# Kernel tuning notes

Hardware: AMD Instinct MI355X
Metric: run time of the kernel (lower is better)

## Reference

```python
import jax, jax.numpy as jnp
import numpy as np

TOPK_POS = 16
TOPK_NEG = 16
EPS = 1e-12  # F.normalize default eps


def _l2norm(x):
    # torch.nn.functional.normalize(p=2, dim=1): x / max(||x||_2, eps)
    n = jnp.sqrt(jnp.sum(x * x, axis=1, keepdims=True))
    return x / jnp.maximum(n, EPS)


def setup_inputs() -> dict:
    key = jax.random.key(0)
    k0, k1, k2, k3, k4 = jax.random.split(key, 5)
    B, I, J, C = 32, 1024, 2048, 1024
    f_rad = jax.random.normal(k0, (B, I), dtype=jnp.float32)
    f_histo = jax.random.normal(k1, (B, J), dtype=jnp.float32)
    rad_mask = jax.random.randint(k2, (B,), 0, 2).astype(bool)
    histo_mask = jax.random.randint(k3, (B,), 0, 2).astype(bool)
    # nn.Linear(in_channels*2, out_channels): weight [C, 2*I], bias [C]
    W = jax.random.normal(k4, (C, 2 * I), dtype=jnp.float32) / np.sqrt(2 * I)
    b = jnp.zeros((C,), dtype=jnp.float32)
    token = jnp.zeros((1, C), dtype=jnp.float32)  # missing_modality_token
    return {"f_rad": f_rad, "f_histo": f_histo, "rad_mask": rad_mask,
            "histo_mask": histo_mask, "W": W, "b": b, "token": token}


def reference(f_rad, f_histo, rad_mask, histo_mask, W, b, token):
    r = _l2norm(f_rad)            # [B, I]
    h = _l2norm(f_histo)          # [B, J]
    sim = jnp.einsum('bi,bj->bij', r, h)  # [B, I, J]
    pos_map = jnp.mean(jax.lax.top_k(sim, TOPK_POS)[0], axis=-1)    # [B, I]
    neg_map = jnp.mean(jax.lax.top_k(-sim, TOPK_NEG)[0], axis=-1)   # [B, I]
    # cat([B,1,I],[B,1,I], dim=1).view(B,-1) == concat(pos, neg) along features
    feat = jnp.concatenate([pos_map, neg_map], axis=1)  # [B, 2I]
    emb = feat @ W.T + b                                 # [B, C]
    # modality_flags = ~torch.min(rad_mask, histo_mask)  (bool AND then NOT)
    flags = (~(rad_mask & histo_mask)).astype(emb.dtype)[:, None]  # [B, 1]
    return emb + token * flags
```

## Files before the change

kernel.cpp:

```cpp
#include <hip/hip_runtime.h>
#include <math.h>

#define NB 32
#define NI 1024
#define NJ 2048
#define NC 1024
#define K2 2048

__global__ __launch_bounds__(256)
void prep_kernel(const float* __restrict__ f_rad,
                 const float* __restrict__ f_histo,
                 const unsigned char* __restrict__ rad_mask,
                 const unsigned char* __restrict__ histo_mask,
                 const float* __restrict__ bias,
                 const float* __restrict__ token,
                 float* __restrict__ F,
                 float* __restrict__ out)
{
    __shared__ float hb[NJ];
    __shared__ float lists[256][16];
    __shared__ float red[256];
    __shared__ float sc[4];

    const int b = blockIdx.x;
    const int t = threadIdx.x;

    float ss = 0.f;
#pragma unroll
    for (int i = 0; i < NJ / 256; ++i) {
        float v = f_histo[b * NJ + t + i * 256];
        hb[t + i * 256] = v;
        ss += v * v;
    }
    red[t] = ss;
    __syncthreads();
#pragma unroll
    for (int s = 128; s > 0; s >>= 1) {
        if (t < s) red[t] += red[t + s];
        __syncthreads();
    }
    if (t == 0) sc[0] = fmaxf(sqrtf(red[0]), 1e-12f);

    for (int pass = 0; pass < 2; ++pass) {
        const float sgn = pass ? -1.f : 1.f;
        float v[16];
#pragma unroll
        for (int i = 0; i < 8; ++i) v[i] = sgn * hb[t + i * 256];
#pragma unroll
        for (int i = 8; i < 16; ++i) v[i] = -__builtin_inff();

#pragma unroll
        for (int a = 0; a < 7; ++a)
#pragma unroll
            for (int c = 0; c < 7 - a; ++c) {
                float x = v[c], y = v[c + 1];
                v[c] = fmaxf(x, y);
                v[c + 1] = fminf(x, y);
            }

        __syncthreads();
#pragma unroll
        for (int i = 0; i < 16; ++i) lists[t][i] = v[i];
        __syncthreads();

#pragma unroll
        for (int s = 128; s >= 1; s >>= 1) {
            if (t < s) {
                float w[16], m[16];
#pragma unroll
                for (int i = 0; i < 16; ++i) w[i] = lists[t + s][i];
#pragma unroll
                for (int i = 0; i < 16; ++i) m[i] = fmaxf(v[i], w[15 - i]);
#pragma unroll
                for (int st = 8; st >= 1; st >>= 1)
#pragma unroll
                    for (int i = 0; i < 16; ++i)
                        if ((i & st) == 0) {
                            float x = m[i], y = m[i + st];
                            m[i] = fmaxf(x, y);
                            m[i + st] = fminf(x, y);
                        }
#pragma unroll
                for (int i = 0; i < 16; ++i) { v[i] = m[i]; lists[t][i] = m[i]; }
            }
            __syncthreads();
        }
        if (t == 0) {
            float s16 = 0.f;
#pragma unroll
            for (int i = 0; i < 16; ++i) s16 += v[i];
            sc[1 + pass] = s16;
        }
    }

    float rv[4];
    float ss2 = 0.f;
#pragma unroll
    for (int i = 0; i < 4; ++i) {
        rv[i] = f_rad[b * NI + t + i * 256];
        ss2 += rv[i] * rv[i];
    }
    __syncthreads();
    red[t] = ss2;
    __syncthreads();
#pragma unroll
    for (int s = 128; s > 0; s >>= 1) {
        if (t < s) red[t] += red[t + s];
        __syncthreads();
    }
    if (t == 0) sc[3] = fmaxf(sqrtf(red[0]), 1e-12f);
    __syncthreads();

    const float hnorm = sc[0];
    const float Hpos = sc[1] / (16.f * hnorm);
    const float Hneg = -sc[2] / (16.f * hnorm);
    const float rnorm = sc[3];

#pragma unroll
    for (int i = 0; i < 4; ++i) {
        float rn = rv[i] / rnorm;
        float p, q;
        if (rn > 0.f) { p = rn * Hpos;  q = -rn * Hneg; }
        else          { p = rn * Hneg;  q = -rn * Hpos; }
        F[b * K2 + t + i * 256]      = p;
        F[b * K2 + NI + t + i * 256] = q;
    }

    const float flag = (rad_mask[b] != 0 && histo_mask[b] != 0) ? 0.f : 1.f;
#pragma unroll
    for (int i = 0; i < NC / 256; ++i) {
        int c = t + i * 256;
        out[b * NC + c] = bias[c] + token[c] * flag;
    }
}

__global__ __launch_bounds__(256)
void gemm_kernel(const float* __restrict__ F,
                 const float* __restrict__ W,
                 float* __restrict__ out)
{
    __shared__ __align__(16) float Fs[NB][512];

    const int t = threadIdx.x;
    const int k0 = blockIdx.y * 1024;
    const int wave = t >> 6;
    const int lane = t & 63;
    const int c0 = blockIdx.x * 8 + wave * 2;

    float acc0[32], acc1[32];
#pragma unroll
    for (int b = 0; b < 32; ++b) { acc0[b] = 0.f; acc1[b] = 0.f; }

    const float4* Wr0 = reinterpret_cast<const float4*>(W + (size_t)c0 * K2 + k0);
    const float4* Wr1 = reinterpret_cast<const float4*>(W + (size_t)(c0 + 1) * K2 + k0);

    for (int ch = 0; ch < 2; ++ch) {
        const int kbase = k0 + ch * 512;
#pragma unroll
        for (int f = 0; f < 16; ++f) {
            int idx = t + f * 256;
            int row = idx >> 7;
            int col = idx & 127;
            reinterpret_cast<float4*>(&Fs[row][0])[col] =
                reinterpret_cast<const float4*>(F + row * K2 + kbase)[col];
        }
        __syncthreads();

#pragma unroll
        for (int r = 0; r < 2; ++r) {
            const int kk4 = r * 64 + lane;
            float4 w0 = Wr0[ch * 128 + kk4];
            float4 w1 = Wr1[ch * 128 + kk4];
#pragma unroll
            for (int b = 0; b < 32; ++b) {
                float4 fv = reinterpret_cast<const float4*>(&Fs[b][0])[kk4];
                acc0[b] = fmaf(fv.x, w0.x, acc0[b]);
                acc0[b] = fmaf(fv.y, w0.y, acc0[b]);
                acc0[b] = fmaf(fv.z, w0.z, acc0[b]);
                acc0[b] = fmaf(fv.w, w0.w, acc0[b]);
                acc1[b] = fmaf(fv.x, w1.x, acc1[b]);
                acc1[b] = fmaf(fv.y, w1.y, acc1[b]);
                acc1[b] = fmaf(fv.z, w1.z, acc1[b]);
                acc1[b] = fmaf(fv.w, w1.w, acc1[b]);
            }
        }
        __syncthreads();
    }

#pragma unroll
    for (int b = 0; b < 32; ++b) {
#pragma unroll
        for (int off = 32; off >= 1; off >>= 1) {
            acc0[b] += __shfl_xor(acc0[b], off, 64);
            acc1[b] += __shfl_xor(acc1[b], off, 64);
        }
    }

    float myval = 0.f;
    const int bsel = lane >> 1;
    const int csel = lane & 1;
#pragma unroll
    for (int b = 0; b < 32; ++b)
        if (bsel == b) myval = csel ? acc1[b] : acc0[b];

    atomicAdd(&out[bsel * NC + c0 + csel], myval);
}

extern "C" void kernel_launch(void* const* d_in, const int* in_sizes, int n_in,
                              void* d_out, int out_size, void* d_ws, size_t ws_size,
                              hipStream_t stream) {
    const float* f_rad       = (const float*)d_in[0];
    const float* f_histo     = (const float*)d_in[1];
    const unsigned char* rm  = (const unsigned char*)d_in[2];
    const unsigned char* hm  = (const unsigned char*)d_in[3];
    const float* W           = (const float*)d_in[4];
    const float* bias        = (const float*)d_in[5];
    const float* token       = (const float*)d_in[6];
    float* out = (float*)d_out;
    float* F   = (float*)d_ws;

    prep_kernel<<<NB, 256, 0, stream>>>(f_rad, f_histo, rm, hm, bias, token, F, out);
    dim3 grid(128, 2);
    gemm_kernel<<<grid, 256, 0, stream>>>(F, W, out);
}
```

Baseline: 101.8 us.

## Fuse top-k passes, use wave-shuffle reductions, drop LDS staging in GEMM

The prep kernel now sorts and merges the positive and negative top-16 lists in one tree pass instead of two. Norm reductions use wave shuffles plus a 4-entry shared array, which removes long chains of __syncthreads. The GEMM kernel no longer stages F in shared memory and reads it straight from global/cache, and the cross-lane reduction uses a butterfly combine that halves the shuffle count. These changes aim to cut barrier and shuffle overhead, at the cost of more register pressure and uncached-through-LDS global reads of F.

```diff
diff --git a/kernel.cpp b/kernel.cpp
--- a/kernel.cpp
+++ b/kernel.cpp
@@ -6,6 +6,24 @@
 #define NJ 2048
 #define NC 1024
 #define K2 2048
+
+__device__ __forceinline__ void merge16(float* __restrict__ v,
+                                        const float* __restrict__ w) {
+    float m[16];
+#pragma unroll
+    for (int i = 0; i < 16; ++i) m[i] = fmaxf(v[i], w[15 - i]);
+#pragma unroll
+    for (int st = 8; st >= 1; st >>= 1)
+#pragma unroll
+        for (int i = 0; i < 16; ++i)
+            if ((i & st) == 0) {
+                float x = m[i], y = m[i + st];
+                m[i] = fmaxf(x, y);
+                m[i + st] = fminf(x, y);
+            }
+#pragma unroll
+    for (int i = 0; i < 16; ++i) v[i] = m[i];
+}
 
 __global__ __launch_bounds__(256)
 void prep_kernel(const float* __restrict__ f_rad,
@@ -17,81 +35,66 @@
                  float* __restrict__ F,
                  float* __restrict__ out)
 {
-    __shared__ float hb[NJ];
-    __shared__ float lists[256][16];
-    __shared__ float red[256];
-    __shared__ float sc[4];
+    __shared__ float listsP[256][16];
+    __shared__ float listsN[256][16];
+    __shared__ float red[4];
 
     const int b = blockIdx.x;
     const int t = threadIdx.x;
-
+    const int wave = t >> 6, lane = t & 63;
+
+    float hv[8];
     float ss = 0.f;
 #pragma unroll
-    for (int i = 0; i < NJ / 256; ++i) {
-        float v = f_histo[b * NJ + t + i * 256];
-        hb[t + i * 256] = v;
-        ss += v * v;
-    }
-    red[t] = ss;
-    __syncthreads();
-#pragma unroll
-    for (int s = 128; s > 0; s >>= 1) {
-        if (t < s) red[t] += red[t + s];
+    for (int i = 0; i < 8; ++i) {
+        hv[i] = f_histo[b * NJ + t + i * 256];
+        ss += hv[i] * hv[i];
+    }
+#pragma unroll
+    for (int off = 1; off < 64; off <<= 1) ss += __shfl_xor(ss, off, 64);
+    if (lane == 0) red[wave] = ss;
+
+    float vp[16], vn[16];
+#pragma unroll
+    for (int i = 0; i < 8; ++i) { vp[i] = hv[i]; vn[i] = -hv[i]; }
+#pragma unroll
+    for (int i = 8; i < 16; ++i) { vp[i] = -INFINITY; vn[i] = -INFINITY; }
+#pragma unroll
+    for (int a = 0; a < 7; ++a)
+#pragma unroll
+        for (int c = 0; c < 7 - a; ++c) {
+            float x = vp[c], y = vp[c + 1];
+            vp[c] = fmaxf(x, y); vp[c + 1] = fminf(x, y);
+            x = vn[c]; y = vn[c + 1];
+            vn[c] = fmaxf(x, y); vn[c + 1] = fminf(x, y);
+        }
+
+    __syncthreads();
+    const float hnorm = fmaxf(sqrtf(red[0] + red[1] + red[2] + red[3]), 1e-12f);
+
+#pragma unroll
+    for (int i = 0; i < 16; ++i) { listsP[t][i] = vp[i]; listsN[t][i] = vn[i]; }
+    __syncthreads();
+
+#pragma unroll
+    for (int s = 128; s >= 1; s >>= 1) {
+        if (t < s) {
+            float wp[16], wn[16];
+#pragma unroll
+            for (int i = 0; i < 16; ++i) { wp[i] = listsP[t + s][i]; wn[i] = listsN[t + s][i]; }
+            merge16(vp, wp);
+            merge16(vn, wn);
+#pragma unroll
+            for (int i = 0; i < 16; ++i) { listsP[t][i] = vp[i]; listsN[t][i] = vn[i]; }
+        }
         __syncthreads();
     }
-    if (t == 0) sc[0] = fmaxf(sqrtf(red[0]), 1e-12f);
-
-    for (int pass = 0; pass < 2; ++pass) {
-        const float sgn = pass ? -1.f : 1.f;
-        float v[16];
-#pragma unroll
-        for (int i = 0; i < 8; ++i) v[i] = sgn * hb[t + i * 256];
-#pragma unroll
-        for (int i = 8; i < 16; ++i) v[i] = -__builtin_inff();
-
-#pragma unroll
-        for (int a = 0; a < 7; ++a)
-#pragma unroll
-            for (int c = 0; c < 7 - a; ++c) {
-                float x = v[c], y = v[c + 1];
-                v[c] = fmaxf(x, y);
-                v[c + 1] = fminf(x, y);
-            }
-
-        __syncthreads();
-#pragma unroll
-        for (int i = 0; i < 16; ++i) lists[t][i] = v[i];
-        __syncthreads();
-
-#pragma unroll
-        for (int s = 128; s >= 1; s >>= 1) {
-            if (t < s) {
-                float w[16], m[16];
-#pragma unroll
-                for (int i = 0; i < 16; ++i) w[i] = lists[t + s][i];
-#pragma unroll
-                for (int i = 0; i < 16; ++i) m[i] = fmaxf(v[i], w[15 - i]);
-#pragma unroll
-                for (int st = 8; st >= 1; st >>= 1)
-#pragma unroll
-                    for (int i = 0; i < 16; ++i)
-                        if ((i & st) == 0) {
-                            float x = m[i], y = m[i + st];
-                            m[i] = fmaxf(x, y);
-                            m[i + st] = fminf(x, y);
-                        }
-#pragma unroll
-                for (int i = 0; i < 16; ++i) { v[i] = m[i]; lists[t][i] = m[i]; }
-            }
-            __syncthreads();
-        }
-        if (t == 0) {
-            float s16 = 0.f;
-#pragma unroll
-            for (int i = 0; i < 16; ++i) s16 += v[i];
-            sc[1 + pass] = s16;
-        }
-    }
+
+    float sumP = 0.f, sumN = 0.f;
+#pragma unroll
+    for (int i = 0; i < 16; ++i) { sumP += listsP[0][i]; sumN += listsN[0][i]; }
+    const float Hpos = sumP / (16.f * hnorm);
+    const float Hneg = -sumN / (16.f * hnorm);
 
     float rv[4];
     float ss2 = 0.f;
@@ -100,21 +103,12 @@
         rv[i] = f_rad[b * NI + t + i * 256];
         ss2 += rv[i] * rv[i];
     }
-    __syncthreads();
-    red[t] = ss2;
-    __syncthreads();
-#pragma unroll
-    for (int s = 128; s > 0; s >>= 1) {
-        if (t < s) red[t] += red[t + s];
-        __syncthreads();
-    }
-    if (t == 0) sc[3] = fmaxf(sqrtf(red[0]), 1e-12f);
-    __syncthreads();
-
-    const float hnorm = sc[0];
-    const float Hpos = sc[1] / (16.f * hnorm);
-    const float Hneg = -sc[2] / (16.f * hnorm);
-    const float rnorm = sc[3];
+#pragma unroll
+    for (int off = 1; off < 64; off <<= 1) ss2 += __shfl_xor(ss2, off, 64);
+    __syncthreads();
+    if (lane == 0) red[wave] = ss2;
+    __syncthreads();
+    const float rnorm = fmaxf(sqrtf(red[0] + red[1] + red[2] + red[3]), 1e-12f);
 
 #pragma unroll
     for (int i = 0; i < 4; ++i) {
@@ -135,75 +129,58 @@
 }
 
 __global__ __launch_bounds__(256)
-void gemm_kernel(const float* __restrict__ F,
+void gemm_kernel(const float4* __restrict__ F4,
                  const float* __restrict__ W,
                  float* __restrict__ out)
 {
-    __shared__ __align__(16) float Fs[NB][512];
-
     const int t = threadIdx.x;
-    const int k0 = blockIdx.y * 1024;
-    const int wave = t >> 6;
-    const int lane = t & 63;
+    const int wave = t >> 6, lane = t & 63;
     const int c0 = blockIdx.x * 8 + wave * 2;
+    const int kb4 = blockIdx.y * 256;
 
     float acc0[32], acc1[32];
 #pragma unroll
     for (int b = 0; b < 32; ++b) { acc0[b] = 0.f; acc1[b] = 0.f; }
 
-    const float4* Wr0 = reinterpret_cast<const float4*>(W + (size_t)c0 * K2 + k0);
-    const float4* Wr1 = reinterpret_cast<const float4*>(W + (size_t)(c0 + 1) * K2 + k0);
-
-    for (int ch = 0; ch < 2; ++ch) {
-        const int kbase = k0 + ch * 512;
-#pragma unroll
-        for (int f = 0; f < 16; ++f) {
-            int idx = t + f * 256;
-            int row = idx >> 7;
-            int col = idx & 127;
-            reinterpret_cast<float4*>(&Fs[row][0])[col] =
-                reinterpret_cast<const float4*>(F + row * K2 + kbase)[col];
+    const float4* Wr0 = reinterpret_cast<const float4*>(W + (size_t)c0 * K2) + kb4;
+    const float4* Wr1 = reinterpret_cast<const float4*>(W + (size_t)(c0 + 1) * K2) + kb4;
+
+#pragma unroll
+    for (int r = 0; r < 4; ++r) {
+        const int kk4 = r * 64 + lane;
+        float4 w0 = Wr0[kk4];
+        float4 w1 = Wr1[kk4];
+#pragma unroll
+        for (int b = 0; b < 32; ++b) {
+            float4 fv = F4[b * 512 + kb4 + kk4];
+            acc0[b] = fmaf(fv.x, w0.x, acc0[b]);
+            acc0[b] = fmaf(fv.y, w0.y, acc0[b]);
+            acc0[b] = fmaf(fv.z, w0.z, acc0[b]);
+            acc0[b] = fmaf(fv.w, w0.w, acc0[b]);
+            acc1[b] = fmaf(fv.x, w1.x, acc1[b]);
+            acc1[b] = fmaf(fv.y, w1.y, acc1[b]);
+            acc1[b] = fmaf(fv.z, w1.z, acc1[b]);
+            acc1[b] = fmaf(fv.w, w1.w, acc1[b]);
         }
-        __syncthreads();
-
-#pragma unroll
-        for (int r = 0; r < 2; ++r) {
-            const int kk4 = r * 64 + lane;
-            float4 w0 = Wr0[ch * 128 + kk4];
-            float4 w1 = Wr1[ch * 128 + kk4];
-#pragma unroll
-            for (int b = 0; b < 32; ++b) {
-                float4 fv = reinterpret_cast<const float4*>(&Fs[b][0])[kk4];
-                acc0[b] = fmaf(fv.x, w0.x, acc0[b]);
-                acc0[b] = fmaf(fv.y, w0.y, acc0[b]);
-                acc0[b] = fmaf(fv.z, w0.z, acc0[b]);
-                acc0[b] = fmaf(fv.w, w0.w, acc0[b]);
-                acc1[b] = fmaf(fv.x, w1.x, acc1[b]);
-                acc1[b] = fmaf(fv.y, w1.y, acc1[b]);
-                acc1[b] = fmaf(fv.z, w1.z, acc1[b]);
-                acc1[b] = fmaf(fv.w, w1.w, acc1[b]);
-            }
-        }
-        __syncthreads();
-    }
-
+    }
+
+    float z[32];
 #pragma unroll
     for (int b = 0; b < 32; ++b) {
-#pragma unroll
-        for (int off = 32; off >= 1; off >>= 1) {
-            acc0[b] += __shfl_xor(acc0[b], off, 64);
-            acc1[b] += __shfl_xor(acc1[b], off, 64);
-        }
-    }
-
+        float a0 = acc0[b] + __shfl_xor(acc0[b], 1, 64);
+        float a1 = acc1[b] + __shfl_xor(acc1[b], 1, 64);
+        z[b] = (lane & 1) ? a1 : a0;
+#pragma unroll
+        for (int off = 2; off < 64; off <<= 1)
+            z[b] += __shfl_xor(z[b], off, 64);
+    }
+    const int bsel = lane >> 1;
     float myval = 0.f;
-    const int bsel = lane >> 1;
-    const int csel = lane & 1;
 #pragma unroll
     for (int b = 0; b < 32; ++b)
-        if (bsel == b) myval = csel ? acc1[b] : acc0[b];
-
-    atomicAdd(&out[bsel * NC + c0 + csel], myval);
+        if (bsel == b) myval = z[b];
+
+    atomicAdd(&out[bsel * NC + c0 + (lane & 1)], myval);
 }
 
 extern "C" void kernel_launch(void* const* d_in, const int* in_sizes, int n_in,
@@ -221,5 +198,5 @@
 
     prep_kernel<<<NB, 256, 0, stream>>>(f_rad, f_histo, rm, hm, bias, token, F, out);
     dim3 grid(128, 2);
-    gemm_kernel<<<grid, 256, 0, stream>>>(F, W, out);
-}
+    gemm_kernel<<<grid, 256, 0, stream>>>((const float4*)F, W, out);
+}
```

Measured after the change: 102.8 us. About the same (+1.0%).
